# Kernel optimization log

Measured on AMD Instinct MI355X. Metric: run time of the kernel, lower is better.

Reference implementation:

```python
import jax, jax.numpy as jnp
import numpy as np

B, S, H, NH = 2, 2048, 1024, 16
HD = H // NH
DFF = 4 * H
EPS = 1e-6


def layer_norm(x, g, b):
    mu = jnp.mean(x, axis=-1, keepdims=True)
    var = jnp.mean(jnp.square(x - mu), axis=-1, keepdims=True)
    return (x - mu) * jax.lax.rsqrt(var + EPS) * g + b


def setup_inputs() -> dict:
    key = jax.random.key(0)
    ks = jax.random.split(key, 10)
    s = 0.02
    return {
        "x": jax.random.normal(ks[0], (B, S, H), jnp.float32),
        "attention_mask": jnp.triu(jnp.ones((S, S), jnp.bool_), k=1),  # causal: True = masked
        "ln1_g": jnp.ones((H,), jnp.float32),
        "ln1_b": jnp.zeros((H,), jnp.float32),
        "ln2_g": jnp.ones((H,), jnp.float32),
        "ln2_b": jnp.zeros((H,), jnp.float32),
        "qkv_w": jax.random.normal(ks[1], (3 * H, H), jnp.float32) * s,
        "out_w": jax.random.normal(ks[2], (H, H), jnp.float32) * s,
        "fc1_w": jax.random.normal(ks[3], (DFF, H), jnp.float32) * s,
        "fc1_b": jnp.zeros((DFF,), jnp.float32),
        "fc2_w": jax.random.normal(ks[4], (H, DFF), jnp.float32) * s,
        "fc2_b": jnp.zeros((H,), jnp.float32),
    }


def reference(x, attention_mask, ln1_g, ln1_b, ln2_g, ln2_b,
              qkv_w, out_w, fc1_w, fc1_b, fc2_w, fc2_b):
    scale = HD ** -0.5
    # --- attention sub-block (pre-norm) ---
    residual = x
    h = layer_norm(x, ln1_g, ln1_b)
    qkv = h @ qkv_w.T                              # [B,S,3H]
    q, k, v = jnp.split(qkv, 3, axis=-1)
    def heads(t):                                  # [B,S,H] -> [B,NH,S,HD]
        return t.reshape(B, S, NH, HD).transpose(0, 2, 1, 3)
    q, k, v = heads(q), heads(k), heads(v)
    scores = jnp.einsum('bhqd,bhkd->bhqk', q, k) * scale
    scores = jnp.where(attention_mask[None, None, :, :], -jnp.inf, scores)
    attn = jax.nn.softmax(scores, axis=-1)
    attn = jnp.nan_to_num(attn, nan=0.0, posinf=0.0, neginf=0.0)
    ctx = jnp.einsum('bhqk,bhkd->bhqd', attn, v)
    ctx = ctx.transpose(0, 2, 1, 3).reshape(B, S, H)
    x = residual + ctx @ out_w.T
    # --- MLP sub-block (pre-norm) ---
    residual = x
    h = layer_norm(x, ln2_g, ln2_b)
    h = jax.nn.gelu(h @ fc1_w.T + fc1_b, approximate=False)
    x = residual + h @ fc2_w.T + fc2_b
    return x
```

## Files before the change

### kernel.cpp

```cpp
#include <hip/hip_runtime.h>
#include <hip/hip_bf16.h>
#include <math.h>

#define B_   2
#define S_   2048
#define H_   1024
#define NH_  16
#define HD_  64
#define DFF_ 4096
#define ROWS (B_*S_)
#define EPS_ 1e-6f
#define NQT  (S_/64)

typedef __hip_bfloat16 bf16;
typedef __attribute__((ext_vector_type(8))) short s8;
typedef __attribute__((ext_vector_type(4))) float f32x4;

__device__ __forceinline__ bf16 to_bf16(float f) { return __float2bfloat16(f); }

#define GLOAD_LDS16(g, l) __builtin_amdgcn_global_load_lds( \
    (const __attribute__((address_space(1))) void*)(g),     \
    (__attribute__((address_space(3))) void*)(l), 16, 0, 0)

__global__ __launch_bounds__(256) void cast_all(const float* __restrict__ w0,
                                                const float* __restrict__ w1,
                                                const float* __restrict__ w2,
                                                const float* __restrict__ w3,
                                                bf16* __restrict__ o0, bf16* __restrict__ o1,
                                                bf16* __restrict__ o2, bf16* __restrict__ o3) {
    size_t u = (size_t)blockIdx.x * 256 + threadIdx.x;
    const size_t n0 = (size_t)3*H_*H_/8, n1 = (size_t)H_*H_/8, n2 = (size_t)DFF_*H_/8;
    const float* src; bf16* dst; size_t base;
    if (u < n0)              { src = w0; dst = o0; base = u; }
    else if (u < n0+n1)      { src = w1; dst = o1; base = u-n0; }
    else if (u < n0+n1+n2)   { src = w2; dst = o2; base = u-n0-n1; }
    else                     { src = w3; dst = o3; base = u-n0-n1-n2; }
    size_t i = base * 8;
    float4 a = *reinterpret_cast<const float4*>(src + i);
    float4 b = *reinterpret_cast<const float4*>(src + i + 4);
    union { bf16 h[8]; s8 v; } uu;
    uu.h[0]=to_bf16(a.x); uu.h[1]=to_bf16(a.y); uu.h[2]=to_bf16(a.z); uu.h[3]=to_bf16(a.w);
    uu.h[4]=to_bf16(b.x); uu.h[5]=to_bf16(b.y); uu.h[6]=to_bf16(b.z); uu.h[7]=to_bf16(b.w);
    *reinterpret_cast<s8*>(dst + i) = uu.v;
}

__global__ __launch_bounds__(256) void ln_bf16(const float* __restrict__ x,
                                               const float* __restrict__ g,
                                               const float* __restrict__ b,
                                               bf16* __restrict__ y) {
    int row = blockIdx.x;
    int t = threadIdx.x;
    float4 v = reinterpret_cast<const float4*>(x + (size_t)row * H_)[t];
    float s  = v.x + v.y + v.z + v.w;
    float ss = v.x*v.x + v.y*v.y + v.z*v.z + v.w*v.w;
    #pragma unroll
    for (int m = 1; m < 64; m <<= 1) {
        s  += __shfl_xor(s,  m, 64);
        ss += __shfl_xor(ss, m, 64);
    }
    __shared__ float ws_s[4], ws_ss[4];
    int wid = t >> 6;
    if ((t & 63) == 0) { ws_s[wid] = s; ws_ss[wid] = ss; }
    __syncthreads();
    s  = ws_s[0] + ws_s[1] + ws_s[2] + ws_s[3];
    ss = ws_ss[0] + ws_ss[1] + ws_ss[2] + ws_ss[3];
    float mu   = s * (1.0f / H_);
    float var  = ss * (1.0f / H_) - mu * mu;
    float rstd = rsqrtf(var + EPS_);
    float4 gv = reinterpret_cast<const float4*>(g)[t];
    float4 bv = reinterpret_cast<const float4*>(b)[t];
    union { bf16 h[4]; short4 sv; } u;
    u.h[0] = to_bf16((v.x - mu) * rstd * gv.x + bv.x);
    u.h[1] = to_bf16((v.y - mu) * rstd * gv.y + bv.y);
    u.h[2] = to_bf16((v.z - mu) * rstd * gv.z + bv.z);
    u.h[3] = to_bf16((v.w - mu) * rstd * gv.w + bv.w);
    *reinterpret_cast<short4*>(y + (size_t)row * H_ + t * 4) = u.sv;
}

template<int EPI, int TN, int OCC, int DB>
__global__ __launch_bounds__(256, OCC) void gemm_bf16(const bf16* __restrict__ A,
                                                      const bf16* __restrict__ Bw,
                                                      bf16* __restrict__ Cb,
                                                      float* __restrict__ Cf,
                                                      bf16* __restrict__ vT,
                                                      const float* __restrict__ bias,
                                                      const float* __restrict__ res,
                                                      int M, int N, int K, int GX) {
    const int NJ = TN / 32;
    const int LA = 128 * 64, LB = TN * 64;
    __shared__ bf16 As[DB * LA];
    __shared__ bf16 Bs[DB * LB];

    int nwg = gridDim.x;
    int ld  = blockIdx.x;
    int wgid = (ld & 7) * (nwg >> 3) + (ld >> 3);
    int by = wgid / GX, bx = wgid % GX;

    int t = threadIdx.x, l = t & 63, w = t >> 6;
    int lr = l & 15, lg = l >> 4;
    size_t bm = (size_t)by * 128, bn = (size_t)bx * TN;

    int sx = lr & 7;
    int scol = ((t & 7) ^ ((t >> 3) & 7)) * 8;
    const bf16* Ag = A  + (bm + (t >> 3)) * K + scol;
    const bf16* Bg = Bw + (bn + (t >> 3)) * K + scol;

    int wr = (w >> 1) << 6, wc = (w & 1) * (TN / 2);

    f32x4 acc[4][NJ];
    const f32x4 z4 = {0.f, 0.f, 0.f, 0.f};
    #pragma unroll
    for (int i = 0; i < 4; ++i)
        #pragma unroll
        for (int j = 0; j < NJ; ++j) acc[i][j] = z4;

    auto STAGE = [&](int buf, int k0) {
        #pragma unroll
        for (int c = 0; c < 4; ++c)
            GLOAD_LDS16(Ag + k0 + (size_t)c * 32 * K, As + buf * LA + w * 512 + c * 2048);
        #pragma unroll
        for (int c = 0; c < NJ; ++c)
            GLOAD_LDS16(Bg + k0 + (size_t)c * 32 * K, Bs + buf * LB + w * 512 + c * 2048);
    };

    auto COMPUTE = [&](int buf) {
        const bf16* Ab = As + buf * LA;
        const bf16* Bb = Bs + buf * LB;
        #pragma unroll
        for (int kk = 0; kk < 64; kk += 32) {
            s8 af[4], bfr[NJ];
            #pragma unroll
            for (int i = 0; i < 4; ++i)
                af[i] = *reinterpret_cast<const s8*>(Ab + (wr + i*16 + lr) * 64
                                                        + ((((kk >> 3) + lg) ^ sx) * 8));
            #pragma unroll
            for (int j = 0; j < NJ; ++j)
                bfr[j] = *reinterpret_cast<const s8*>(Bb + (wc + j*16 + lr) * 64
                                                         + ((((kk >> 3) + lg) ^ sx) * 8));
            #pragma unroll
            for (int i = 0; i < 4; ++i)
                #pragma unroll
                for (int j = 0; j < NJ; ++j)
                    acc[i][j] = __builtin_amdgcn_mfma_f32_16x16x32_bf16(af[i], bfr[j], acc[i][j], 0, 0, 0);
        }
    };

    if (DB == 1) {
        for (int k0 = 0; k0 < K; k0 += 64) {
            STAGE(0, k0);
            asm volatile("s_waitcnt vmcnt(0)" ::: "memory");
            __syncthreads();
            COMPUTE(0);
            __syncthreads();
        }
    } else {
        const int NT = K >> 6;
        STAGE(0, 0);
        asm volatile("s_waitcnt vmcnt(0)" ::: "memory");
        __syncthreads();
        int cur = 0;
        for (int it = 0; it < NT; ++it) {
            if (it + 1 < NT) STAGE(cur ^ 1, (it + 1) << 6);
            COMPUTE(cur);
            asm volatile("s_waitcnt vmcnt(0)" ::: "memory");
            __syncthreads();
            cur ^= 1;
        }
    }

    float bias_v[NJ];
    if (EPI == 2 || EPI == 3) {
        #pragma unroll
        for (int j = 0; j < NJ; ++j) bias_v[j] = bias[bn + wc + j*16 + lr];
    }
    #pragma unroll
    for (int i = 0; i < 4; ++i) {
        #pragma unroll
        for (int q = 0; q < 4; ++q) {
            size_t rg = bm + wr + i*16 + lg*4 + q;
            #pragma unroll
            for (int j = 0; j < NJ; ++j) {
                size_t cg = bn + wc + j*16 + lr;
                float v = acc[i][j][q];
                if (EPI == 0) {
                    if (cg < 2048) {
                        Cb[rg * N + cg] = to_bf16(v);
                    } else {
                        int hd = (int)cg - 2048;
                        int hh = hd >> 6, d = hd & 63;
                        int bb = (int)(rg >> 11), sq = (int)(rg & 2047);
                        vT[(((size_t)(bb * NH_ + hh)) * HD_ + d) * S_ + sq] = to_bf16(v);
                    }
                } else if (EPI == 1) {
                    Cf[rg * N + cg] = v + res[rg * N + cg];
                } else if (EPI == 2) {
                    float u = v + bias_v[j];
                    u = 0.5f * u * (1.0f + erff(u * 0.70710678118654752f));
                    Cb[rg * N + cg] = to_bf16(u);
                } else {
                    Cf[rg * N + cg] = v + bias_v[j] + res[rg * N + cg];
                }
            }
        }
    }
}

__global__ __launch_bounds__(512, 2) void gemm256_fc1(const bf16* __restrict__ A,
                                                      const bf16* __restrict__ Bw,
                                                      bf16* __restrict__ C,
                                                      const float* __restrict__ bias,
                                                      int M, int N, int K) {
    __shared__ bf16 As[2][256 * 64];
    __shared__ bf16 Bs[2][256 * 64];

    int nwg = gridDim.x;
    int ld  = blockIdx.x;
    int wgid = (ld & 7) * (nwg >> 3) + (ld >> 3);
    int GX = N >> 8;
    int by = wgid / GX, bx = wgid % GX;
    size_t bm = (size_t)by << 8, bn = (size_t)bx << 8;

    int t = threadIdx.x, l = t & 63, w = t >> 6;
    int lr = l & 15, lg = l >> 4;
    int wr2 = w >> 2, wc2 = w & 3;
    int sx = lr & 7;

    int scol = ((l & 7) ^ (l >> 3)) * 8;
    const bf16* Ag = A  + (bm + w * 8 + (l >> 3)) * K + scol;
    const bf16* Bg = Bw + (bn + w * 8 + (l >> 3)) * K + scol;

    f32x4 acc[8][4];
    const f32x4 z4 = {0.f, 0.f, 0.f, 0.f};
    #pragma unroll
    for (int i = 0; i < 8; ++i)
        #pragma unroll
        for (int j = 0; j < 4; ++j) acc[i][j] = z4;

    auto STAGE = [&](int buf, int k0) {
        #pragma unroll
        for (int s = 0; s < 4; ++s)
            GLOAD_LDS16(Ag + k0 + (size_t)s * 64 * K, &As[buf][s * 4096 + w * 512]);
        #pragma unroll
        for (int s = 0; s < 4; ++s)
            GLOAD_LDS16(Bg + k0 + (size_t)s * 64 * K, &Bs[buf][s * 4096 + w * 512]);
    };

    auto KSLICE = [&](int buf, int kx) {
        s8 af[8], bfr[4];
        #pragma unroll
        for (int m4 = 0; m4 < 8; ++m4) {
            int R = wr2 * 128 + m4 * 16 + lr;
            af[m4] = *reinterpret_cast<const s8*>(&As[buf][R * 64 + (((kx << 2) + lg) ^ sx) * 8]);
        }
        #pragma unroll
        for (int n2 = 0; n2 < 4; ++n2) {
            int R = wc2 * 64 + n2 * 16 + lr;
            bfr[n2] = *reinterpret_cast<const s8*>(&Bs[buf][R * 64 + (((kx << 2) + lg) ^ sx) * 8]);
        }
        __builtin_amdgcn_s_setprio(1);
        #pragma unroll
        for (int m4 = 0; m4 < 8; ++m4)
            #pragma unroll
            for (int n2 = 0; n2 < 4; ++n2)
                acc[m4][n2] = __builtin_amdgcn_mfma_f32_16x16x32_bf16(af[m4], bfr[n2],
                                                                      acc[m4][n2], 0, 0, 0);
        __builtin_amdgcn_s_setprio(0);
        __builtin_amdgcn_sched_barrier(0);
    };

    const int NT = K >> 6;
    STAGE(0, 0);
    STAGE(1, 64);
    for (int tt = 0; tt < NT; ++tt) {
        int buf = tt & 1;
        if (tt + 1 < NT) { asm volatile("s_waitcnt vmcnt(8)" ::: "memory"); }
        else             { asm volatile("s_waitcnt vmcnt(0)" ::: "memory"); }
        __builtin_amdgcn_s_barrier();
        KSLICE(buf, 0);
        KSLICE(buf, 1);
        __builtin_amdgcn_s_barrier();
        if (tt + 2 < NT) STAGE(buf, (tt + 2) << 6);
    }

    float bv[4];
    int colb = (int)bn + wc2 * 64;
    #pragma unroll
    for (int n = 0; n < 4; ++n) bv[n] = bias[colb + n * 16 + lr];
    #pragma unroll
    for (int m = 0; m < 8; ++m) {
        #pragma unroll
        for (int q = 0; q < 4; ++q) {
            size_t rg = bm + wr2 * 128 + m * 16 + lg * 4 + q;
            #pragma unroll
            for (int n = 0; n < 4; ++n) {
                float u = acc[m][n][q] + bv[n];
                u = 0.5f * u * (1.0f + erff(u * 0.70710678118654752f));
                C[rg * N + colb + n * 16 + lr] = to_bf16(u);
            }
        }
    }
}

#define KVB 128

__device__ __forceinline__ s8 scale_q8(s8 v) {
    union { s8 v; bf16 h[8]; } u; u.v = v;
    #pragma unroll
    for (int e = 0; e < 8; ++e)
        u.h[e] = to_bf16(__bfloat162float(u.h[e]) * 0.125f);
    return u.v;
}

__device__ __forceinline__ void attn_qtile(int qt, int h, int b, int t,
                                           const bf16* __restrict__ qkvb,
                                           const bf16* __restrict__ vT,
                                           bf16* __restrict__ ctx,
                                           bf16* Ks, bf16* Vt, bf16* Pw) {
    int l = t & 63, w = t >> 6, lr = l & 15, lg = l >> 4;
    int qb = qt * 64;

    const bf16* qp = qkvb + ((size_t)(b * S_) + qb + w * 16 + lr) * (3 * H_) + h * HD_;
    s8 qf0 = scale_q8(*reinterpret_cast<const s8*>(qp + lg * 8));
    s8 qf1 = scale_q8(*reinterpret_cast<const s8*>(qp + 32 + lg * 8));

    const f32x4 z4 = {0.f, 0.f, 0.f, 0.f};
    f32x4 oacc[4];
    #pragma unroll
    for (int n = 0; n < 4; ++n) oacc[n] = z4;
    float lsum[4] = {0.f, 0.f, 0.f, 0.f};

    int krow = t >> 1, kcol = (t & 1) * 32;
    int vd   = t >> 2, vk = (t & 3) * 8;
    const bf16* kbase = qkvb + ((size_t)(b * S_) + krow) * (3 * H_) + H_ + h * HD_ + kcol;
    const bf16* vbase = vT + ((size_t)((b * NH_ + h) * HD_) + vd) * S_ + vk;

    int nt = (qt >> 1) + 1;
    s8 k0 = *reinterpret_cast<const s8*>(kbase);
    s8 k1 = *reinterpret_cast<const s8*>(kbase + 8);
    s8 k2 = *reinterpret_cast<const s8*>(kbase + 16);
    s8 k3 = *reinterpret_cast<const s8*>(kbase + 24);
    s8 v0 = *reinterpret_cast<const s8*>(vbase);
    s8 v1 = *reinterpret_cast<const s8*>(vbase + 32);
    s8 v2 = *reinterpret_cast<const s8*>(vbase + 64);
    s8 v3 = *reinterpret_cast<const s8*>(vbase + 96);

    for (int it = 0; it < nt; ++it) {
        int kvb0 = it * KVB;
        __syncthreads();
        *reinterpret_cast<s8*>(&Ks[krow * 72 + kcol])      = k0;
        *reinterpret_cast<s8*>(&Ks[krow * 72 + kcol + 8])  = k1;
        *reinterpret_cast<s8*>(&Ks[krow * 72 + kcol + 16]) = k2;
        *reinterpret_cast<s8*>(&Ks[krow * 72 + kcol + 24]) = k3;
        *reinterpret_cast<s8*>(&Vt[vd * 136 + vk])         = v0;
        *reinterpret_cast<s8*>(&Vt[vd * 136 + vk + 32])    = v1;
        *reinterpret_cast<s8*>(&Vt[vd * 136 + vk + 64])    = v2;
        *reinterpret_cast<s8*>(&Vt[vd * 136 + vk + 96])    = v3;
        int nx = (it + 1 < nt) ? kvb0 + KVB : kvb0;
        const bf16* kn = kbase + (size_t)nx * (3 * H_);
        const bf16* vn = vbase + nx;
        k0 = *reinterpret_cast<const s8*>(kn);
        k1 = *reinterpret_cast<const s8*>(kn + 8);
        k2 = *reinterpret_cast<const s8*>(kn + 16);
        k3 = *reinterpret_cast<const s8*>(kn + 24);
        v0 = *reinterpret_cast<const s8*>(vn);
        v1 = *reinterpret_cast<const s8*>(vn + 32);
        v2 = *reinterpret_cast<const s8*>(vn + 64);
        v3 = *reinterpret_cast<const s8*>(vn + 96);
        __syncthreads();

        f32x4 sa[8];
        __builtin_amdgcn_s_setprio(1);
        #pragma unroll
        for (int n = 0; n < 8; ++n) {
            f32x4 zz = z4;
            s8 kf0 = *reinterpret_cast<const s8*>(&Ks[(n*16 + lr) * 72 + lg * 8]);
            s8 kf1 = *reinterpret_cast<const s8*>(&Ks[(n*16 + lr) * 72 + 32 + lg * 8]);
            zz = __builtin_amdgcn_mfma_f32_16x16x32_bf16(qf0, kf0, zz, 0, 0, 0);
            zz = __builtin_amdgcn_mfma_f32_16x16x32_bf16(qf1, kf1, zz, 0, 0, 0);
            sa[n] = zz;
        }
        __builtin_amdgcn_s_setprio(0);

        bool mask = (kvb0 + KVB > qb);
        #pragma unroll
        for (int q = 0; q < 4; ++q) {
            int qrow = qb + w*16 + lg*4 + q;
            #pragma unroll
            for (int n = 0; n < 8; ++n) {
                float s = sa[n][q];
                if (mask) {
                    int col = kvb0 + n*16 + lr;
                    s = (col <= qrow) ? s : -1e30f;
                }
                float e = __expf(s);
                lsum[q] += e;
                Pw[(lg*4 + q) * 136 + n*16 + lr] = to_bf16(e);
            }
        }
        asm volatile("s_waitcnt lgkmcnt(0)" ::: "memory");
        __builtin_amdgcn_sched_barrier(0);

        __builtin_amdgcn_s_setprio(1);
        #pragma unroll
        for (int ks = 0; ks < 4; ++ks) {
            s8 pf = *reinterpret_cast<const s8*>(&Pw[lr * 136 + ks*32 + lg * 8]);
            #pragma unroll
            for (int n = 0; n < 4; ++n) {
                s8 vf = *reinterpret_cast<const s8*>(&Vt[(n*16 + lr) * 136 + ks*32 + lg * 8]);
                oacc[n] = __builtin_amdgcn_mfma_f32_16x16x32_bf16(pf, vf, oacc[n], 0, 0, 0);
            }
        }
        __builtin_amdgcn_s_setprio(0);
    }

    #pragma unroll
    for (int m = 1; m < 16; m <<= 1) {
        #pragma unroll
        for (int q = 0; q < 4; ++q) lsum[q] += __shfl_xor(lsum[q], m, 64);
    }

    #pragma unroll
    for (int q = 0; q < 4; ++q) {
        float inv = 1.0f / lsum[q];
        size_t row = (size_t)(b * S_) + qb + w * 16 + lg * 4 + q;
        #pragma unroll
        for (int n = 0; n < 4; ++n)
            ctx[row * H_ + h * HD_ + n * 16 + lr] = to_bf16(oacc[n][q] * inv);
    }
}

__global__ __launch_bounds__(256) void attn_mfma(const bf16* __restrict__ qkvb,
                                                 const bf16* __restrict__ vT,
                                                 bf16* __restrict__ ctx) {
    __shared__ bf16 Ks[KVB * 72];
    __shared__ bf16 Vt[64 * 136];
    __shared__ bf16 Pw[4][16 * 136];
    int t = threadIdx.x;
    int w = t >> 6;
    int lin = blockIdx.x;
    int nl  = (lin & 7) * 64 + (lin >> 3);
    int qp  = nl & 15;
    int h   = (nl >> 4) & 15;
    int b   = nl >> 8;
    attn_qtile(qp,           h, b, t, qkvb, vT, ctx, Ks, Vt, Pw[w]);
    attn_qtile(NQT - 1 - qp, h, b, t, qkvb, vT, ctx, Ks, Vt, Pw[w]);
}

extern "C" void kernel_launch(void* const* d_in, const int* in_sizes, int n_in,
                              void* d_out, int out_size, void* d_ws, size_t ws_size,
                              hipStream_t stream) {
    const float* x     = (const float*)d_in[0];
    const float* ln1_g = (const float*)d_in[2];
    const float* ln1_b = (const float*)d_in[3];
    const float* ln2_g = (const float*)d_in[4];
    const float* ln2_b = (const float*)d_in[5];
    const float* qkv_w = (const float*)d_in[6];
    const float* out_w = (const float*)d_in[7];
    const float* fc1_w = (const float*)d_in[8];
    const float* fc1_b = (const float*)d_in[9];
    const float* fc2_w = (const float*)d_in[10];
    const float* fc2_b = (const float*)d_in[11];
    float* out = (float*)d_out;

    bf16* w_qkv  = (bf16*)d_ws;
    bf16* w_out  = w_qkv  + (size_t)3*H_*H_;
    bf16* w_fc1  = w_out  + (size_t)H_*H_;
    bf16* w_fc2  = w_fc1  + (size_t)DFF_*H_;
    bf16* h_bf   = w_fc2  + (size_t)H_*DFF_;
    bf16* qkv_bf = h_bf   + (size_t)ROWS*H_;
    bf16* vTb    = qkv_bf + (size_t)ROWS*3*H_;
    bf16* ctx_bf = vTb    + (size_t)B_*NH_*HD_*S_;
    bf16* ff_bf  = ctx_bf + (size_t)ROWS*H_;

    cast_all<<<6144, 256, 0, stream>>>(qkv_w, out_w, fc1_w, fc2_w,
                                       w_qkv, w_out, w_fc1, w_fc2);

    ln_bf16<<<ROWS, 256, 0, stream>>>(x, ln1_g, ln1_b, h_bf);
    gemm_bf16<0,128,2,1><<<32 * 24, 256, 0, stream>>>(h_bf, w_qkv, qkv_bf, nullptr, vTb,
                                                      nullptr, nullptr, ROWS, 3*H_, H_, 24);
    attn_mfma<<<512, 256, 0, stream>>>(qkv_bf, vTb, ctx_bf);
    gemm_bf16<1,64,3,2><<<32 * 16, 256, 0, stream>>>(ctx_bf, w_out, nullptr, out, nullptr,
                                                     nullptr, x, ROWS, H_, H_, 16);
    ln_bf16<<<ROWS, 256, 0, stream>>>(out, ln2_g, ln2_b, h_bf);
    gemm256_fc1<<<256, 512, 0, stream>>>(h_bf, w_fc1, ff_bf, fc1_b, ROWS, DFF_, H_);
    gemm_bf16<3,64,3,2><<<32 * 16, 256, 0, stream>>>(ff_bf, w_fc2, nullptr, out, nullptr,
                                                     fc2_b, out, ROWS, H_, DFF_, 16);
}
```

Before: 231.3 us.

## Shrink fc1 GEMM tile to 256x128 and drop LDS double buffering

The fc1 GEMM moves from 256x256 tiles with double-buffered LDS and prefetch two k-steps ahead to 256x128 tiles with a single LDS buffer. The grid grows from 256 to 512 workgroups and the launch bound rises to 4 waves per SIMD. The aim is to cut LDS and register use so more workgroups stay resident and all CUs get work. Each k-step now does load, wait, sync, then compute with no overlap between loading and compute inside a block, and each loaded A tile is reused across fewer output columns.

```diff
diff --git a/kernel.cpp b/kernel.cpp
--- a/kernel.cpp
+++ b/kernel.cpp
@@ -205,94 +205,89 @@
     }
 }
 
-__global__ __launch_bounds__(512, 2) void gemm256_fc1(const bf16* __restrict__ A,
+__global__ __launch_bounds__(512, 4) void gemm_fc1_v2(const bf16* __restrict__ A,
                                                       const bf16* __restrict__ Bw,
                                                       bf16* __restrict__ C,
                                                       const float* __restrict__ bias,
                                                       int M, int N, int K) {
-    __shared__ bf16 As[2][256 * 64];
-    __shared__ bf16 Bs[2][256 * 64];
+    __shared__ bf16 As[256 * 64];
+    __shared__ bf16 Bs[128 * 64];
 
     int nwg = gridDim.x;
     int ld  = blockIdx.x;
     int wgid = (ld & 7) * (nwg >> 3) + (ld >> 3);
-    int GX = N >> 8;
+    int GX = N >> 7;
     int by = wgid / GX, bx = wgid % GX;
-    size_t bm = (size_t)by << 8, bn = (size_t)bx << 8;
+    size_t bm = (size_t)by << 8, bn = (size_t)bx << 7;
 
     int t = threadIdx.x, l = t & 63, w = t >> 6;
     int lr = l & 15, lg = l >> 4;
     int wr2 = w >> 2, wc2 = w & 3;
     int sx = lr & 7;
 
-    int scol = ((l & 7) ^ (l >> 3)) * 8;
-    const bf16* Ag = A  + (bm + w * 8 + (l >> 3)) * K + scol;
-    const bf16* Bg = Bw + (bn + w * 8 + (l >> 3)) * K + scol;
-
-    f32x4 acc[8][4];
+    int scol = ((t & 7) ^ ((t >> 3) & 7)) * 8;
+    const bf16* Ag = A  + (bm + (t >> 3)) * K + scol;
+    const bf16* Bg = Bw + (bn + (t >> 3)) * K + scol;
+
+    f32x4 acc[8][2];
     const f32x4 z4 = {0.f, 0.f, 0.f, 0.f};
     #pragma unroll
     for (int i = 0; i < 8; ++i)
         #pragma unroll
-        for (int j = 0; j < 4; ++j) acc[i][j] = z4;
-
-    auto STAGE = [&](int buf, int k0) {
-        #pragma unroll
-        for (int s = 0; s < 4; ++s)
-            GLOAD_LDS16(Ag + k0 + (size_t)s * 64 * K, &As[buf][s * 4096 + w * 512]);
-        #pragma unroll
-        for (int s = 0; s < 4; ++s)
-            GLOAD_LDS16(Bg + k0 + (size_t)s * 64 * K, &Bs[buf][s * 4096 + w * 512]);
+        for (int j = 0; j < 2; ++j) acc[i][j] = z4;
+
+    auto STAGE = [&](int k0) {
+        #pragma unroll
+        for (int c = 0; c < 4; ++c)
+            GLOAD_LDS16(Ag + k0 + (size_t)c * 64 * K, As + c * 4096 + w * 512);
+        #pragma unroll
+        for (int c = 0; c < 2; ++c)
+            GLOAD_LDS16(Bg + k0 + (size_t)c * 64 * K, Bs + c * 4096 + w * 512);
     };
 
-    auto KSLICE = [&](int buf, int kx) {
-        s8 af[8], bfr[4];
+    auto KSLICE = [&](int kx) {
+        s8 af[8], bfr[2];
         #pragma unroll
         for (int m4 = 0; m4 < 8; ++m4) {
             int R = wr2 * 128 + m4 * 16 + lr;
-            af[m4] = *reinterpret_cast<const s8*>(&As[buf][R * 64 + (((kx << 2) + lg) ^ sx) * 8]);
-        }
-        #pragma unroll
-        for (int n2 = 0; n2 < 4; ++n2) {
-            int R = wc2 * 64 + n2 * 16 + lr;
-            bfr[n2] = *reinterpret_cast<const s8*>(&Bs[buf][R * 64 + (((kx << 2) + lg) ^ sx) * 8]);
+            af[m4] = *reinterpret_cast<const s8*>(&As[R * 64 + (((kx << 2) + lg) ^ sx) * 8]);
+        }
+        #pragma unroll
+        for (int n2 = 0; n2 < 2; ++n2) {
+            int R = wc2 * 32 + n2 * 16 + lr;
+            bfr[n2] = *reinterpret_cast<const s8*>(&Bs[R * 64 + (((kx << 2) + lg) ^ sx) * 8]);
         }
         __builtin_amdgcn_s_setprio(1);
         #pragma unroll
         for (int m4 = 0; m4 < 8; ++m4)
             #pragma unroll
-            for (int n2 = 0; n2 < 4; ++n2)
+            for (int n2 = 0; n2 < 2; ++n2)
                 acc[m4][n2] = __builtin_amdgcn_mfma_f32_16x16x32_bf16(af[m4], bfr[n2],
                                                                       acc[m4][n2], 0, 0, 0);
         __builtin_amdgcn_s_setprio(0);
         __builtin_amdgcn_sched_barrier(0);
     };
 
-    const int NT = K >> 6;
-    STAGE(0, 0);
-    STAGE(1, 64);
-    for (int tt = 0; tt < NT; ++tt) {
-        int buf = tt & 1;
-        if (tt + 1 < NT) { asm volatile("s_waitcnt vmcnt(8)" ::: "memory"); }
-        else             { asm volatile("s_waitcnt vmcnt(0)" ::: "memory"); }
-        __builtin_amdgcn_s_barrier();
-        KSLICE(buf, 0);
-        KSLICE(buf, 1);
-        __builtin_amdgcn_s_barrier();
-        if (tt + 2 < NT) STAGE(buf, (tt + 2) << 6);
-    }
-
-    float bv[4];
-    int colb = (int)bn + wc2 * 64;
-    #pragma unroll
-    for (int n = 0; n < 4; ++n) bv[n] = bias[colb + n * 16 + lr];
+    for (int k0 = 0; k0 < K; k0 += 64) {
+        STAGE(k0);
+        asm volatile("s_waitcnt vmcnt(0)" ::: "memory");
+        __syncthreads();
+        KSLICE(0);
+        KSLICE(1);
+        __syncthreads();
+    }
+
+    float bv[2];
+    int colb = (int)bn + wc2 * 32;
+    #pragma unroll
+    for (int n = 0; n < 2; ++n) bv[n] = bias[colb + n * 16 + lr];
     #pragma unroll
     for (int m = 0; m < 8; ++m) {
         #pragma unroll
         for (int q = 0; q < 4; ++q) {
             size_t rg = bm + wr2 * 128 + m * 16 + lg * 4 + q;
             #pragma unroll
-            for (int n = 0; n < 4; ++n) {
+            for (int n = 0; n < 2; ++n) {
                 float u = acc[m][n][q] + bv[n];
                 u = 0.5f * u * (1.0f + erff(u * 0.70710678118654752f));
                 C[rg * N + colb + n * 16 + lr] = to_bf16(u);
@@ -482,7 +477,7 @@
     gemm_bf16<1,64,3,2><<<32 * 16, 256, 0, stream>>>(ctx_bf, w_out, nullptr, out, nullptr,
                                                      nullptr, x, ROWS, H_, H_, 16);
     ln_bf16<<<ROWS, 256, 0, stream>>>(out, ln2_g, ln2_b, h_bf);
-    gemm256_fc1<<<256, 512, 0, stream>>>(h_bf, w_fc1, ff_bf, fc1_b, ROWS, DFF_, H_);
+    gemm_fc1_v2<<<512, 512, 0, stream>>>(h_bf, w_fc1, ff_bf, fc1_b, ROWS, DFF_, H_);
     gemm_bf16<3,64,3,2><<<32 * 16, 256, 0, stream>>>(ff_bf, w_fc2, nullptr, out, nullptr,
                                                      fc2_b, out, ROWS, H_, DFF_, 16);
 }
```

Measured after the change: 222.9 us. 3.6% less time.
